# Kernel optimization log

Hardware: AMD Instinct MI355X
Metric: run time of the kernel (lower is better)

The kernel has to match this reference:

```python
import jax, jax.numpy as jnp
import numpy as np

BLOCK_SIZE = 1024
OUTLIER_SIGMA = 3.0
OUT_FEATURES = 11008
IN_FEATURES = 4096
TOKENS = 64


def _quantize_mixed_np(W):
    """Faithful numpy port of quantize_mixed (BLOCK_SIZE divides numel exactly here)."""
    flat = W.astype(np.float32).reshape(-1)
    nb = flat.size // BLOCK_SIZE
    blocks = flat.reshape(nb, BLOCK_SIZE)
    mu = blocks.mean(axis=1, keepdims=True)
    sig = np.maximum(blocks.std(axis=1, ddof=1, keepdims=True), 1e-8)  # torch.std is unbiased
    outlier = np.abs(blocks - mu) > OUTLIER_SIGMA * sig
    abs_max = np.maximum(np.abs(np.where(outlier, 0.0, blocks)).max(axis=1), 1e-8)
    scales = (abs_max / 127.0).astype(np.float16)
    q = np.clip(np.round(blocks / abs_max[:, None] * 127.0), -127, 127).astype(np.int8)
    all_pos = np.arange(nb, dtype=np.int64)[:, None] * BLOCK_SIZE + np.arange(BLOCK_SIZE, dtype=np.int64)[None, :]
    int8_data = q[~outlier]                      # row-major == torch order
    fp16_data = blocks[outlier].astype(np.float16)
    int8_pos = all_pos[~outlier].astype(np.int32)
    fp16_pos = all_pos[outlier].astype(np.int32)
    block_idx = np.nonzero(~outlier)[0].astype(np.int32)  # block index per int8 value
    return int8_data, fp16_data, scales, int8_pos, fp16_pos, block_idx


def setup_inputs() -> dict:
    key = jax.random.key(0)
    k_x, k_b = jax.random.split(key)
    rng = np.random.default_rng(0)
    W = (rng.standard_normal((OUT_FEATURES, IN_FEATURES)) * 0.02).astype(np.float32)
    int8_data, fp16_data, scales, int8_pos, fp16_pos, block_idx = _quantize_mixed_np(W)
    x = jax.random.normal(k_x, (TOKENS, IN_FEATURES), dtype=jnp.float16)
    bias = jax.random.normal(k_b, (OUT_FEATURES,), dtype=jnp.float16) * jnp.float16(0.02)
    return {
        "x": x,
        "int8_data": jnp.asarray(int8_data),
        "fp16_data": jnp.asarray(fp16_data),
        "scales": jnp.asarray(scales),
        "bias": bias,
        "int8_pos": jnp.asarray(int8_pos),
        "fp16_pos": jnp.asarray(fp16_pos),
        "block_idx": jnp.asarray(block_idx),
    }


def reference(x, int8_data, fp16_data, scales, bias, int8_pos, fp16_pos, block_idx):
    out_features = bias.shape[0]
    in_features = x.shape[1]
    numel = out_features * in_features  # divisible by BLOCK_SIZE for these dims
    # dequantize_mixed: scatter fp16 outliers and dequantized int8 values into flat fp16 buffer
    flat = jnp.zeros((numel,), dtype=jnp.float16)
    flat = flat.at[fp16_pos].set(fp16_data)
    flat = flat.at[int8_pos].set(int8_data.astype(jnp.float16) * scales[block_idx])
    W = flat.reshape(out_features, in_features)
    # F.linear(x, W, bias) in fp16
    return jnp.dot(x.astype(jnp.float16), W.T) + bias
```

## Files before the change

kernel.cpp:

```cpp
#include <hip/hip_runtime.h>
#include <hip/hip_fp16.h>

#define TOK   64
#define INF   4096
#define OUTF  11008
#define NUMEL (OUTF * INF)
#define NSLC  (NUMEL / 64)
#define NBLK  (OUTF / 16)
#define KSPL  8
#define OUTN  (TOK * OUTF)

typedef __attribute__((ext_vector_type(8))) _Float16 half8;
typedef __attribute__((ext_vector_type(4))) _Float16 half4;
typedef __attribute__((ext_vector_type(4))) float floatx4;
typedef __attribute__((ext_vector_type(4), aligned(4))) int int4u;
typedef __attribute__((ext_vector_type(4))) int int4a;

#define BPAD 520

__global__ __launch_bounds__(256) void precompute_kernel(
    const float* __restrict__ x, const int* __restrict__ fppos, int nf,
    _Float16* __restrict__ x16, int* __restrict__ meta) {
  const int t = blockIdx.x * 256 + threadIdx.x;
  if (t < (TOK * INF) / 4) {
    const floatx4 f = *(const floatx4*)&x[t * 4];
    half4 h;
    h[0] = (_Float16)f[0]; h[1] = (_Float16)f[1];
    h[2] = (_Float16)f[2]; h[3] = (_Float16)f[3];
    *(half4*)&x16[t * 4] = h;
  }
  if (t < NSLC) {
    const int target = t << 6;
    int lo = 0, hi = nf;
    while (lo < hi) {
      const int mid = (lo + hi) >> 1;
      if (fppos[mid] < target) lo = mid + 1; else hi = mid;
    }
    unsigned long long mask = 0ull;
    int j = lo;
    while (j < nf) {
      const int d = fppos[j] - target;
      if (d >= 64) break;
      mask |= 1ull << d;
      ++j;
    }
    int4a mv;
    mv[0] = lo;
    mv[1] = (int)(unsigned)(mask & 0xffffffffu);
    mv[2] = (int)(unsigned)(mask >> 32);
    mv[3] = 0;
    *(int4a*)&meta[t * 4] = mv;
  }
}

__device__ __forceinline__ half8 dq_slot_meta(
    const int p0, const int c0, const unsigned mlo, const unsigned mhi,
    const float s, const int* __restrict__ i8,
    const float* __restrict__ fpdat, const int n8) {
  const int off = p0 & 63;
  const unsigned m8 = 0xffu & (off < 32 ? (mlo >> off) : (mhi >> (off - 32)));
  const unsigned bl = (off >= 32) ? mlo : (mlo & ((1u << off) - 1u));
  const unsigned bh = (off >= 32) ? (mhi & ((1u << (off - 32)) - 1u)) : 0u;
  const int lt = __popc(bl) + __popc(bh);
  const int i0 = p0 - c0 - lt;
  const int f  = (int)m8;

  float ov[8];
#pragma unroll
  for (int e = 0; e < 8; ++e) ov[e] = 0.f;
  if (f) {
    int fi = c0 + lt;
#pragma unroll
    for (int e = 0; e < 8; ++e) {
      if ((f >> e) & 1) { ov[e] = fpdat[fi]; ++fi; }
    }
  }

  half8 oh;
  if (i0 + 8 <= n8) {
    int l[8];
    *(int4u*)&l[0] = *(const int4u*)&i8[i0];
    *(int4u*)&l[4] = *(const int4u*)&i8[i0 + 4];
    if (f == 0) {
#pragma unroll
      for (int e = 0; e < 8; ++e) oh[e] = (_Float16)((float)l[e] * s);
    } else {
      int q = 0;
#pragma unroll
      for (int e = 0; e < 8; ++e) {
        const int flg = (f >> e) & 1;
        int lv = l[0];
#pragma unroll
        for (int qq = 1; qq < 8; ++qq) lv = (q == qq) ? l[qq] : lv;
        oh[e] = flg ? (_Float16)ov[e] : (_Float16)((float)lv * s);
        q += 1 - flg;
      }
    }
  } else {
    int c = 0;
    const int m = n8 - 1;
#pragma unroll
    for (int e = 0; e < 8; ++e) {
      const int flg = (f >> e) & 1;
      int idx = i0 + e - c;
      idx = idx < 0 ? 0 : (idx > m ? m : idx);
      oh[e] = flg ? (_Float16)ov[e] : (_Float16)((float)i8[idx] * s);
      c += flg;
    }
  }
  return oh;
}

__global__ __launch_bounds__(256) void gemm_fused(
    const _Float16* __restrict__ x16,
    const int* __restrict__ i8, const float* __restrict__ fpdat,
    const float* __restrict__ scales, const int* __restrict__ meta,
    float* __restrict__ part, const int n8) {
  __shared__ __attribute__((aligned(16))) char smem[16 * BPAD * 2];
  _Float16 (* __restrict__ Bt)[BPAD] = (_Float16 (*)[BPAD])smem;
  float* red = (float*)smem;

  const int tid  = threadIdx.x;
  const int wave = tid >> 6;
  const int lane = tid & 63;
  const int quad = lane >> 4;
  const int ln   = lane & 15;
  const int nt   = blockIdx.x >> 3;
  const int kq   = blockIdx.x & 7;
  const int n0   = nt * 16;
  const int kbas = kq * 512;

  int p0v[4], c0v[4];
  unsigned mlov[4], mhiv[4];
  float sv[4];
#pragma unroll
  for (int i = 0; i < 4; ++i) {
    const int slot = i * 256 + tid;
    const int r    = slot >> 6;
    const int k8   = slot & 63;
    const int p0   = (n0 + r) * INF + kbas + k8 * 8;
    const int4a mv = *(const int4a*)&meta[(p0 >> 6) * 4];
    p0v[i] = p0;
    c0v[i] = mv[0];
    mlov[i] = (unsigned)mv[1];
    mhiv[i] = (unsigned)mv[2];
    sv[i]  = scales[p0 >> 10];
  }

#pragma unroll
  for (int i = 0; i < 4; ++i) {
    const int slot = i * 256 + tid;
    const int r    = slot >> 6;
    const int k8   = slot & 63;
    const half8 oh = dq_slot_meta(p0v[i], c0v[i], mlov[i], mhiv[i], sv[i],
                                  i8, fpdat, n8);
    *(half8*)&Bt[r][k8 * 8] = oh;
  }
  __syncthreads();

  const int ko0 = wave * 128 + quad * 8;
  const _Float16* ap = &x16[ln * INF + kbas + ko0];
  const _Float16* bp = &Bt[ln][ko0];

  floatx4 acc0 = {0,0,0,0}, acc1 = {0,0,0,0}, acc2 = {0,0,0,0}, acc3 = {0,0,0,0};
#pragma unroll
  for (int st = 0; st < 4; ++st) {
    const int ko = st * 32;
    const half8 bh = *(const half8*)&bp[ko];
    const half8 a0 = *(const half8*)&ap[ko];
    const half8 a1 = *(const half8*)&ap[16 * INF + ko];
    const half8 a2 = *(const half8*)&ap[32 * INF + ko];
    const half8 a3 = *(const half8*)&ap[48 * INF + ko];
    acc0 = __builtin_amdgcn_mfma_f32_16x16x32_f16(a0, bh, acc0, 0, 0, 0);
    acc1 = __builtin_amdgcn_mfma_f32_16x16x32_f16(a1, bh, acc1, 0, 0, 0);
    acc2 = __builtin_amdgcn_mfma_f32_16x16x32_f16(a2, bh, acc2, 0, 0, 0);
    acc3 = __builtin_amdgcn_mfma_f32_16x16x32_f16(a3, bh, acc3, 0, 0, 0);
  }
  __syncthreads();

  const int mb = quad * 4;
#pragma unroll
  for (int i = 0; i < 4; ++i) red[wave * 1024 + (mb + i)      * 16 + ln] = acc0[i];
#pragma unroll
  for (int i = 0; i < 4; ++i) red[wave * 1024 + (16 + mb + i) * 16 + ln] = acc1[i];
#pragma unroll
  for (int i = 0; i < 4; ++i) red[wave * 1024 + (32 + mb + i) * 16 + ln] = acc2[i];
#pragma unroll
  for (int i = 0; i < 4; ++i) red[wave * 1024 + (48 + mb + i) * 16 + ln] = acc3[i];
  __syncthreads();

  float* pp = &part[(size_t)kq * OUTN];
#pragma unroll
  for (int c2 = 0; c2 < 4; ++c2) {
    const int cell = tid + c2 * 256;
    const int mm = cell >> 4, nn = cell & 15;
    pp[mm * OUTF + n0 + nn] =
        red[cell] + red[1024 + cell] + red[2048 + cell] + red[3072 + cell];
  }
}

__global__ __launch_bounds__(256) void reduce_kernel(
    const float* __restrict__ part, const float* __restrict__ bias,
    float* __restrict__ out) {
  const int t  = blockIdx.x * 256 + threadIdx.x;
  const int i4 = t * 4;
  floatx4 a = *(const floatx4*)&part[i4];
#pragma unroll
  for (int k = 1; k < KSPL; ++k) {
    const floatx4 b = *(const floatx4*)&part[(size_t)k * OUTN + i4];
    a[0] += b[0]; a[1] += b[1]; a[2] += b[2]; a[3] += b[3];
  }
  const int nn = i4 % OUTF;
  const floatx4 bb = *(const floatx4*)&bias[nn];
  a[0] += bb[0]; a[1] += bb[1]; a[2] += bb[2]; a[3] += bb[3];
  *(floatx4*)&out[i4] = a;
}

extern "C" void kernel_launch(void* const* d_in, const int* in_sizes, int n_in,
                              void* d_out, int out_size, void* d_ws,
                              size_t ws_size, hipStream_t stream) {
  const float* x      = (const float*)d_in[0];
  const int*   i8     = (const int*)d_in[1];
  const float* fpdat  = (const float*)d_in[2];
  const float* scales = (const float*)d_in[3];
  const float* bias   = (const float*)d_in[4];
  const int*   fppos  = (const int*)d_in[6];

  char* wsp = (char*)d_ws;
  _Float16* x16  = (_Float16*)wsp;
  int*      meta = (int*)(wsp + (size_t)TOK * INF * sizeof(_Float16));
  float*    part = (float*)(wsp + (size_t)TOK * INF * sizeof(_Float16)
                                + (size_t)NSLC * 16);
  float*    out  = (float*)d_out;

  const int n8 = in_sizes[1];
  const int nf = in_sizes[2];

  precompute_kernel<<<NSLC / 256, 256, 0, stream>>>(x, fppos, nf, x16, meta);
  gemm_fused<<<NBLK * KSPL, 256, 0, stream>>>(x16, i8, fpdat, scales, meta,
                                              part, n8);
  reduce_kernel<<<OUTN / (4 * 256), 256, 0, stream>>>(part, bias, out);
}
```

Before: 446.0 us.

## Replace split-K with full-K loop double-buffering dequant and fusing bias epilogue

The GEMM kernel now covers the whole K dimension in one block per 16-column tile. It loops over eight 512-wide chunks with double-buffered LDS, prefetching metadata and int8 loads for later chunks while the MFMAs run on the current one. This drops the partial-sum buffer and the separate reduce kernel, adding bias in the epilogue. In exchange the grid shrinks from 5504 to 688 blocks, which lowers parallelism on a GPU with many CUs and leans on in-block pipelining to hide latency.

```diff
diff --git a/kernel.cpp b/kernel.cpp
--- a/kernel.cpp
+++ b/kernel.cpp
@@ -7,8 +7,7 @@
 #define NUMEL (OUTF * INF)
 #define NSLC  (NUMEL / 64)
 #define NBLK  (OUTF / 16)
-#define KSPL  8
-#define OUTN  (TOK * OUTF)
+#define NCH   8
 
 typedef __attribute__((ext_vector_type(8))) _Float16 half8;
 typedef __attribute__((ext_vector_type(4))) _Float16 half4;
@@ -53,23 +52,27 @@
   }
 }
 
-__device__ __forceinline__ half8 dq_slot_meta(
-    const int p0, const int c0, const unsigned mlo, const unsigned mhi,
-    const float s, const int* __restrict__ i8,
-    const float* __restrict__ fpdat, const int n8) {
+__device__ __forceinline__ void meta_window(const int p0, const int4a mv,
+                                            int& i0, unsigned& m8) {
+  const unsigned mlo = (unsigned)mv[1];
+  const unsigned mhi = (unsigned)mv[2];
   const int off = p0 & 63;
-  const unsigned m8 = 0xffu & (off < 32 ? (mlo >> off) : (mhi >> (off - 32)));
+  m8 = 0xffu & (off < 32 ? (mlo >> off) : (mhi >> (off - 32)));
   const unsigned bl = (off >= 32) ? mlo : (mlo & ((1u << off) - 1u));
   const unsigned bh = (off >= 32) ? (mhi & ((1u << (off - 32)) - 1u)) : 0u;
-  const int lt = __popc(bl) + __popc(bh);
-  const int i0 = p0 - c0 - lt;
-  const int f  = (int)m8;
-
+  i0 = p0 - mv[0] - (__popc(bl) + __popc(bh));
+}
+
+__device__ __forceinline__ half8 finish_slot(
+    const unsigned m8, const int i0, const int p0, const float s,
+    const int (&l)[8], const int* __restrict__ i8,
+    const float* __restrict__ fpdat, const int n8) {
+  const int f = (int)m8;
   float ov[8];
 #pragma unroll
   for (int e = 0; e < 8; ++e) ov[e] = 0.f;
   if (f) {
-    int fi = c0 + lt;
+    int fi = p0 - i0;
 #pragma unroll
     for (int e = 0; e < 8; ++e) {
       if ((f >> e) & 1) { ov[e] = fpdat[fi]; ++fi; }
@@ -78,9 +81,6 @@
 
   half8 oh;
   if (i0 + 8 <= n8) {
-    int l[8];
-    *(int4u*)&l[0] = *(const int4u*)&i8[i0];
-    *(int4u*)&l[4] = *(const int4u*)&i8[i0 + 4];
     if (f == 0) {
 #pragma unroll
       for (int e = 0; e < 8; ++e) oh[e] = (_Float16)((float)l[e] * s);
@@ -112,12 +112,12 @@
 }
 
 __global__ __launch_bounds__(256) void gemm_fused(
-    const _Float16* __restrict__ x16,
-    const int* __restrict__ i8, const float* __restrict__ fpdat,
-    const float* __restrict__ scales, const int* __restrict__ meta,
-    float* __restrict__ part, const int n8) {
-  __shared__ __attribute__((aligned(16))) char smem[16 * BPAD * 2];
-  _Float16 (* __restrict__ Bt)[BPAD] = (_Float16 (*)[BPAD])smem;
+    const _Float16* __restrict__ x16, const int* __restrict__ i8,
+    const float* __restrict__ fpdat, const float* __restrict__ scales,
+    const int* __restrict__ meta, const float* __restrict__ bias,
+    float* __restrict__ out, const int n8) {
+  __shared__ __attribute__((aligned(16))) char smem[2 * 16 * BPAD * 2];
+  _Float16 (* __restrict__ Bt)[16][BPAD] = (_Float16 (*)[16][BPAD])smem;
   float* red = (float*)smem;
 
   const int tid  = threadIdx.x;
@@ -125,58 +125,113 @@
   const int lane = tid & 63;
   const int quad = lane >> 4;
   const int ln   = lane & 15;
-  const int nt   = blockIdx.x >> 3;
-  const int kq   = blockIdx.x & 7;
-  const int n0   = nt * 16;
-  const int kbas = kq * 512;
-
-  int p0v[4], c0v[4];
-  unsigned mlov[4], mhiv[4];
-  float sv[4];
+  const int n0   = blockIdx.x << 4;
+
+  int rL[4], k8o[4];
 #pragma unroll
   for (int i = 0; i < 4; ++i) {
     const int slot = i * 256 + tid;
-    const int r    = slot >> 6;
-    const int k8   = slot & 63;
-    const int p0   = (n0 + r) * INF + kbas + k8 * 8;
-    const int4a mv = *(const int4a*)&meta[(p0 >> 6) * 4];
-    p0v[i] = p0;
-    c0v[i] = mv[0];
-    mlov[i] = (unsigned)mv[1];
-    mhiv[i] = (unsigned)mv[2];
-    sv[i]  = scales[p0 >> 10];
-  }
-
-#pragma unroll
-  for (int i = 0; i < 4; ++i) {
-    const int slot = i * 256 + tid;
-    const int r    = slot >> 6;
-    const int k8   = slot & 63;
-    const half8 oh = dq_slot_meta(p0v[i], c0v[i], mlov[i], mhiv[i], sv[i],
-                                  i8, fpdat, n8);
-    *(half8*)&Bt[r][k8 * 8] = oh;
+    rL[i]  = slot >> 6;
+    k8o[i] = (slot & 63) * 8;
+  }
+
+  int4a  mreg[2][4];
+  float  sreg[2][4];
+  int    lreg[4][8];
+  int    i0v[4];
+  unsigned m8v[4];
+
+#pragma unroll
+  for (int i = 0; i < 4; ++i) {
+    const int p0 = (n0 + rL[i]) * INF + k8o[i];
+    mreg[0][i] = *(const int4a*)&meta[(p0 >> 6) * 4];
+    sreg[0][i] = scales[p0 >> 10];
+  }
+#pragma unroll
+  for (int i = 0; i < 4; ++i) {
+    const int p0 = (n0 + rL[i]) * INF + 512 + k8o[i];
+    mreg[1][i] = *(const int4a*)&meta[(p0 >> 6) * 4];
+    sreg[1][i] = scales[p0 >> 10];
+  }
+#pragma unroll
+  for (int i = 0; i < 4; ++i) {
+    const int p0 = (n0 + rL[i]) * INF + k8o[i];
+    meta_window(p0, mreg[0][i], i0v[i], m8v[i]);
+    if (i0v[i] + 8 <= n8) {
+      *(int4u*)&lreg[i][0] = *(const int4u*)&i8[i0v[i]];
+      *(int4u*)&lreg[i][4] = *(const int4u*)&i8[i0v[i] + 4];
+    }
+  }
+#pragma unroll
+  for (int i = 0; i < 4; ++i) {
+    const int p0 = (n0 + rL[i]) * INF + k8o[i];
+    const half8 oh = finish_slot(m8v[i], i0v[i], p0, sreg[0][i], lreg[i],
+                                 i8, fpdat, n8);
+    *(half8*)&Bt[0][rL[i]][k8o[i]] = oh;
   }
   __syncthreads();
 
-  const int ko0 = wave * 128 + quad * 8;
-  const _Float16* ap = &x16[ln * INF + kbas + ko0];
-  const _Float16* bp = &Bt[ln][ko0];
-
   floatx4 acc0 = {0,0,0,0}, acc1 = {0,0,0,0}, acc2 = {0,0,0,0}, acc3 = {0,0,0,0};
-#pragma unroll
-  for (int st = 0; st < 4; ++st) {
-    const int ko = st * 32;
-    const half8 bh = *(const half8*)&bp[ko];
-    const half8 a0 = *(const half8*)&ap[ko];
-    const half8 a1 = *(const half8*)&ap[16 * INF + ko];
-    const half8 a2 = *(const half8*)&ap[32 * INF + ko];
-    const half8 a3 = *(const half8*)&ap[48 * INF + ko];
-    acc0 = __builtin_amdgcn_mfma_f32_16x16x32_f16(a0, bh, acc0, 0, 0, 0);
-    acc1 = __builtin_amdgcn_mfma_f32_16x16x32_f16(a1, bh, acc1, 0, 0, 0);
-    acc2 = __builtin_amdgcn_mfma_f32_16x16x32_f16(a2, bh, acc2, 0, 0, 0);
-    acc3 = __builtin_amdgcn_mfma_f32_16x16x32_f16(a3, bh, acc3, 0, 0, 0);
-  }
-  __syncthreads();
+
+#pragma unroll
+  for (int c = 0; c < NCH; ++c) {
+    const int cur = c & 1;
+
+    if (c + 1 < NCH) {
+      const int bk = (c + 1) & 1;
+#pragma unroll
+      for (int i = 0; i < 4; ++i) {
+        const int p0 = (n0 + rL[i]) * INF + (c + 1) * 512 + k8o[i];
+        meta_window(p0, mreg[bk][i], i0v[i], m8v[i]);
+        if (i0v[i] + 8 <= n8) {
+          *(int4u*)&lreg[i][0] = *(const int4u*)&i8[i0v[i]];
+          *(int4u*)&lreg[i][4] = *(const int4u*)&i8[i0v[i] + 4];
+        }
+      }
+      if (c + 2 < NCH) {
+        const int bk2 = c & 1;
+#pragma unroll
+        for (int i = 0; i < 4; ++i) {
+          const int p0 = (n0 + rL[i]) * INF + (c + 2) * 512 + k8o[i];
+          mreg[bk2][i] = *(const int4a*)&meta[(p0 >> 6) * 4];
+          sreg[bk2][i] = scales[p0 >> 10];
+        }
+      }
+    }
+
+    {
+      const _Float16* ap = &x16[ln * INF + c * 512 + wave * 128 + quad * 8];
+      const _Float16* bp = &Bt[cur][ln][wave * 128 + quad * 8];
+#pragma unroll
+      for (int st = 0; st < 4; ++st) {
+        const int ko = st * 32;
+        const half8 bh = *(const half8*)&bp[ko];
+        const half8 a0 = *(const half8*)&ap[ko];
+        const half8 a1 = *(const half8*)&ap[16 * INF + ko];
+        const half8 a2 = *(const half8*)&ap[32 * INF + ko];
+        const half8 a3 = *(const half8*)&ap[48 * INF + ko];
+        acc0 = __builtin_amdgcn_mfma_f32_16x16x32_f16(a0, bh, acc0, 0, 0, 0);
+        acc1 = __builtin_amdgcn_mfma_f32_16x16x32_f16(a1, bh, acc1, 0, 0, 0);
+        acc2 = __builtin_amdgcn_mfma_f32_16x16x32_f16(a2, bh, acc2, 0, 0, 0);
+        acc3 = __builtin_amdgcn_mfma_f32_16x16x32_f16(a3, bh, acc3, 0, 0, 0);
+      }
+    }
+
+    if (c + 1 < NCH) {
+      const int bk = (c + 1) & 1;
+      half8 oh[4];
+#pragma unroll
+      for (int i = 0; i < 4; ++i) {
+        const int p0 = (n0 + rL[i]) * INF + (c + 1) * 512 + k8o[i];
+        oh[i] = finish_slot(m8v[i], i0v[i], p0, sreg[bk][i], lreg[i],
+                            i8, fpdat, n8);
+      }
+#pragma unroll
+      for (int i = 0; i < 4; ++i)
+        *(half8*)&Bt[bk][rL[i]][k8o[i]] = oh[i];
+      __syncthreads();
+    }
+  }
 
   const int mb = quad * 4;
 #pragma unroll
@@ -189,31 +244,14 @@
   for (int i = 0; i < 4; ++i) red[wave * 1024 + (48 + mb + i) * 16 + ln] = acc3[i];
   __syncthreads();
 
-  float* pp = &part[(size_t)kq * OUTN];
 #pragma unroll
   for (int c2 = 0; c2 < 4; ++c2) {
     const int cell = tid + c2 * 256;
     const int mm = cell >> 4, nn = cell & 15;
-    pp[mm * OUTF + n0 + nn] =
-        red[cell] + red[1024 + cell] + red[2048 + cell] + red[3072 + cell];
-  }
-}
-
-__global__ __launch_bounds__(256) void reduce_kernel(
-    const float* __restrict__ part, const float* __restrict__ bias,
-    float* __restrict__ out) {
-  const int t  = blockIdx.x * 256 + threadIdx.x;
-  const int i4 = t * 4;
-  floatx4 a = *(const floatx4*)&part[i4];
-#pragma unroll
-  for (int k = 1; k < KSPL; ++k) {
-    const floatx4 b = *(const floatx4*)&part[(size_t)k * OUTN + i4];
-    a[0] += b[0]; a[1] += b[1]; a[2] += b[2]; a[3] += b[3];
-  }
-  const int nn = i4 % OUTF;
-  const floatx4 bb = *(const floatx4*)&bias[nn];
-  a[0] += bb[0]; a[1] += bb[1]; a[2] += bb[2]; a[3] += bb[3];
-  *(floatx4*)&out[i4] = a;
+    const float v = red[cell] + red[1024 + cell] + red[2048 + cell]
+                  + red[3072 + cell] + bias[n0 + nn];
+    out[mm * OUTF + n0 + nn] = v;
+  }
 }
 
 extern "C" void kernel_launch(void* const* d_in, const int* in_sizes, int n_in,
@@ -229,15 +267,12 @@
   char* wsp = (char*)d_ws;
   _Float16* x16  = (_Float16*)wsp;
   int*      meta = (int*)(wsp + (size_t)TOK * INF * sizeof(_Float16));
-  float*    part = (float*)(wsp + (size_t)TOK * INF * sizeof(_Float16)
-                                + (size_t)NSLC * 16);
   float*    out  = (float*)d_out;
 
   const int n8 = in_sizes[1];
   const int nf = in_sizes[2];
 
   precompute_kernel<<<NSLC / 256, 256, 0, stream>>>(x, fppos, nf, x16, meta);
-  gemm_fused<<<NBLK * KSPL, 256, 0, stream>>>(x16, i8, fpdat, scales, meta,
-                                              part, n8);
-  reduce_kernel<<<OUTN / (4 * 256), 256, 0, stream>>>(part, bias, out);
-}
+  gemm_fused<<<NBLK, 256, 0, stream>>>(x16, i8, fpdat, scales, meta, bias,
+                                       out, n8);
+}
```

Result: slower. 539.6 us (+21.0%).

## Split dequant into separate kernel writing MFMA-ready fp16 weights, halve K-split

Applied to the files above, without the earlier changes.

Moves weight dequantization out of the fused GEMM into its own kernel that writes a full fp16 weight buffer, laid out so each MFMA lane loads its B fragment directly from global memory. The GEMM kernel then skips the LDS staging and barrier, and the K-split drops from 8 to 4, so each block does more MFMA steps and there are fewer partial sums to reduce. The cost is an extra round trip of the roughly 90MB fp16 weight buffer through global memory and one more kernel launch.

```diff
diff --git a/kernel.cpp b/kernel.cpp
--- a/kernel.cpp
+++ b/kernel.cpp
@@ -7,7 +7,7 @@
 #define NUMEL (OUTF * INF)
 #define NSLC  (NUMEL / 64)
 #define NBLK  (OUTF / 16)
-#define KSPL  8
+#define KSPL  4
 #define OUTN  (TOK * OUTF)
 
 typedef __attribute__((ext_vector_type(8))) _Float16 half8;
@@ -15,8 +15,6 @@
 typedef __attribute__((ext_vector_type(4))) float floatx4;
 typedef __attribute__((ext_vector_type(4), aligned(4))) int int4u;
 typedef __attribute__((ext_vector_type(4))) int int4a;
-
-#define BPAD 520
 
 __global__ __launch_bounds__(256) void precompute_kernel(
     const float* __restrict__ x, const int* __restrict__ fppos, int nf,
@@ -111,72 +109,63 @@
   return oh;
 }
 
-__global__ __launch_bounds__(256) void gemm_fused(
-    const _Float16* __restrict__ x16,
+__global__ __launch_bounds__(256) void dequant_kernel(
     const int* __restrict__ i8, const float* __restrict__ fpdat,
     const float* __restrict__ scales, const int* __restrict__ meta,
-    float* __restrict__ part, const int n8) {
-  __shared__ __attribute__((aligned(16))) char smem[16 * BPAD * 2];
-  _Float16 (* __restrict__ Bt)[BPAD] = (_Float16 (*)[BPAD])smem;
-  float* red = (float*)smem;
+    _Float16* __restrict__ Wt, const int n8) {
+  const int tid  = threadIdx.x;
+  const int wave = tid >> 6;
+  const int lane = tid & 63;
+  const int r    = lane >> 2;
+  const int q    = lane & 3;
+  const int nt   = blockIdx.x >> 3;
+  const int kcg  = ((blockIdx.x & 7) << 4) + (wave << 2);
+  const int row  = (nt << 4) + r;
+  const float s  = scales[row * 4 + (kcg >> 5)];
+
+#pragma unroll
+  for (int j = 0; j < 4; ++j) {
+    const int kc = kcg + j;
+    const int p0 = (row << 12) + (kc << 5) + (q << 3);
+    const int4a mv = *(const int4a*)&meta[(p0 >> 6) * 4];
+    const half8 oh = dq_slot_meta(p0, mv[0], (unsigned)mv[1], (unsigned)mv[2],
+                                  s, i8, fpdat, n8);
+    *(half8*)&Wt[(size_t)((nt * 128 + kc) * 64 + q * 16 + r) * 8] = oh;
+  }
+}
+
+__global__ __launch_bounds__(256) void gemm_kernel(
+    const _Float16* __restrict__ x16, const _Float16* __restrict__ Wt,
+    float* __restrict__ part) {
+  __shared__ float red[4 * 64 * 16];
 
   const int tid  = threadIdx.x;
   const int wave = tid >> 6;
   const int lane = tid & 63;
   const int quad = lane >> 4;
   const int ln   = lane & 15;
-  const int nt   = blockIdx.x >> 3;
-  const int kq   = blockIdx.x & 7;
-  const int n0   = nt * 16;
-  const int kbas = kq * 512;
-
-  int p0v[4], c0v[4];
-  unsigned mlov[4], mhiv[4];
-  float sv[4];
-#pragma unroll
-  for (int i = 0; i < 4; ++i) {
-    const int slot = i * 256 + tid;
-    const int r    = slot >> 6;
-    const int k8   = slot & 63;
-    const int p0   = (n0 + r) * INF + kbas + k8 * 8;
-    const int4a mv = *(const int4a*)&meta[(p0 >> 6) * 4];
-    p0v[i] = p0;
-    c0v[i] = mv[0];
-    mlov[i] = (unsigned)mv[1];
-    mhiv[i] = (unsigned)mv[2];
-    sv[i]  = scales[p0 >> 10];
-  }
-
-#pragma unroll
-  for (int i = 0; i < 4; ++i) {
-    const int slot = i * 256 + tid;
-    const int r    = slot >> 6;
-    const int k8   = slot & 63;
-    const half8 oh = dq_slot_meta(p0v[i], c0v[i], mlov[i], mhiv[i], sv[i],
-                                  i8, fpdat, n8);
-    *(half8*)&Bt[r][k8 * 8] = oh;
-  }
-  __syncthreads();
-
-  const int ko0 = wave * 128 + quad * 8;
-  const _Float16* ap = &x16[ln * INF + kbas + ko0];
-  const _Float16* bp = &Bt[ln][ko0];
+  const int nt   = blockIdx.x >> 2;
+  const int kq   = blockIdx.x & 3;
+  const int n0   = nt << 4;
+  const int kb   = kq * 1024 + wave * 256;
+  const int kc0  = kq * 32 + wave * 8;
+
+  const _Float16* ap = &x16[ln * INF + kb + quad * 8];
+  const _Float16* bp = &Wt[((size_t)(nt * 128 + kc0) * 64 + lane) * 8];
 
   floatx4 acc0 = {0,0,0,0}, acc1 = {0,0,0,0}, acc2 = {0,0,0,0}, acc3 = {0,0,0,0};
 #pragma unroll
-  for (int st = 0; st < 4; ++st) {
-    const int ko = st * 32;
-    const half8 bh = *(const half8*)&bp[ko];
-    const half8 a0 = *(const half8*)&ap[ko];
-    const half8 a1 = *(const half8*)&ap[16 * INF + ko];
-    const half8 a2 = *(const half8*)&ap[32 * INF + ko];
-    const half8 a3 = *(const half8*)&ap[48 * INF + ko];
+  for (int st = 0; st < 8; ++st) {
+    const half8 bh = *(const half8*)&bp[st * 512];
+    const half8 a0 = *(const half8*)&ap[st * 32];
+    const half8 a1 = *(const half8*)&ap[16 * INF + st * 32];
+    const half8 a2 = *(const half8*)&ap[32 * INF + st * 32];
+    const half8 a3 = *(const half8*)&ap[48 * INF + st * 32];
     acc0 = __builtin_amdgcn_mfma_f32_16x16x32_f16(a0, bh, acc0, 0, 0, 0);
     acc1 = __builtin_amdgcn_mfma_f32_16x16x32_f16(a1, bh, acc1, 0, 0, 0);
     acc2 = __builtin_amdgcn_mfma_f32_16x16x32_f16(a2, bh, acc2, 0, 0, 0);
     acc3 = __builtin_amdgcn_mfma_f32_16x16x32_f16(a3, bh, acc3, 0, 0, 0);
   }
-  __syncthreads();
 
   const int mb = quad * 4;
 #pragma unroll
@@ -231,13 +220,16 @@
   int*      meta = (int*)(wsp + (size_t)TOK * INF * sizeof(_Float16));
   float*    part = (float*)(wsp + (size_t)TOK * INF * sizeof(_Float16)
                                 + (size_t)NSLC * 16);
+  _Float16* Wt   = (_Float16*)(wsp + (size_t)TOK * INF * sizeof(_Float16)
+                                   + (size_t)NSLC * 16
+                                   + (size_t)KSPL * OUTN * sizeof(float));
   float*    out  = (float*)d_out;
 
   const int n8 = in_sizes[1];
   const int nf = in_sizes[2];
 
   precompute_kernel<<<NSLC / 256, 256, 0, stream>>>(x, fppos, nf, x16, meta);
-  gemm_fused<<<NBLK * KSPL, 256, 0, stream>>>(x16, i8, fpdat, scales, meta,
-                                              part, n8);
+  dequant_kernel<<<NBLK * 8, 256, 0, stream>>>(i8, fpdat, scales, meta, Wt, n8);
+  gemm_kernel<<<NBLK * KSPL, 256, 0, stream>>>(x16, Wt, part);
   reduce_kernel<<<OUTN / (4 * 256), 256, 0, stream>>>(part, bias, out);
 }
```

New measurement: 487.7 us. +9.3%, slower.
